# Kernel tuning notes

Hardware: AMD Instinct MI355X
Metric: run time of the kernel (lower is better)

## Reference

```python
import jax, jax.numpy as jnp
import numpy as np

QLEN, BSZ, HID, NH, HD = 512, 8, 1024, 16, 64
PLEN = 2 * QLEN
SCALE = 1.0 / (HD ** 0.5)
BIG_NUM = 1e30
EPS = 1e-5


def _rel_shift(x, klen):
    # x: [b, n, i, j] -> shifted [b, n, i, klen], same raw-reshape trick as torch.
    b, n, i, j = x.shape
    x = x.reshape(b, n, j, i)[:, :, 1:, :]
    x = x.reshape(b, n, i, j - 1)
    return x[:, :, :, :klen]


def setup_inputs() -> dict:
    key = jax.random.key(0)
    ks = jax.random.split(key, 12)
    s = jnp.float32(0.02)
    return {
        "hidden_states": jax.random.normal(ks[0], (QLEN, BSZ, HID), jnp.float32),
        "position_embed": jax.random.normal(ks[1], (PLEN, BSZ, HID), jnp.float32),
        "segment_embed": jax.random.uniform(ks[2], (QLEN, QLEN, BSZ, 2), jnp.float32),
        "attn_mask": jnp.zeros((QLEN, QLEN, BSZ, 1), jnp.float32),
        "q": jax.random.normal(ks[3], (HID, NH, HD), jnp.float32) * s,
        "k": jax.random.normal(ks[4], (HID, NH, HD), jnp.float32) * s,
        "v": jax.random.normal(ks[5], (HID, NH, HD), jnp.float32) * s,
        "r": jax.random.normal(ks[6], (HID, NH, HD), jnp.float32) * s,
        "o": jax.random.normal(ks[7], (HID, NH, HD), jnp.float32) * s,
        "r_w_bias": jax.random.normal(ks[8], (NH, HD), jnp.float32) * s,
        "r_r_bias": jax.random.normal(ks[9], (NH, HD), jnp.float32) * s,
        "r_s_bias": jax.random.normal(ks[10], (NH, HD), jnp.float32) * s,
        "seg_mat": jax.random.normal(ks[11], (2, NH, HD), jnp.float32) * s,
        "ln_gamma": jnp.ones((HID,), jnp.float32),
        "ln_beta": jnp.zeros((HID,), jnp.float32),
    }


def reference(hidden_states, position_embed, segment_embed, attn_mask,
              q, k, v, r, o, r_w_bias, r_r_bias, r_s_bias, seg_mat,
              ln_gamma, ln_beta):
    query = jnp.einsum('ibh,hnd->ibnd', hidden_states, q)
    key_ = jnp.einsum('ibh,hnd->ibnd', hidden_states, k)
    value = jnp.einsum('ibh,hnd->ibnd', hidden_states, v)
    key_r = jnp.einsum('ibh,hnd->ibnd', position_embed, r)

    # content score
    ac = jnp.einsum('ibnd,jbnd->bnij', query + r_w_bias, key_)
    # relative position score with rel_shift
    bd = jnp.einsum('ibnd,jbnd->bnij', query + r_r_bias, key_r)
    bd = _rel_shift(bd, ac.shape[3])
    # segment score
    ef = jnp.einsum('ibnd,snd->ibns', query + r_s_bias, seg_mat)
    ef = jnp.einsum('ijbs,ibns->bnij', segment_embed, ef)

    attn_score = (ac + bd + ef) * SCALE
    attn_score = attn_score - BIG_NUM * jnp.transpose(attn_mask, (2, 3, 0, 1))
    attn_prob = jax.nn.softmax(attn_score, axis=-1)  # dropout is identity in eval

    attn_out = jnp.einsum('bnij,jbnd->ibnd', attn_prob, value)
    attn_out = jnp.einsum('ibnd,hnd->ibh', attn_out, o)

    x = attn_out + hidden_states
    mu = jnp.mean(x, axis=-1, keepdims=True)
    var = jnp.mean((x - mu) ** 2, axis=-1, keepdims=True)
    return (x - mu) * jax.lax.rsqrt(var + EPS) * ln_gamma + ln_beta
```

## Files before the change

kernel.cpp:

```cpp
#include <hip/hip_runtime.h>
#include <hip/hip_bf16.h>

#define I_LEN 512
#define BSZ   8
#define HIDN  1024
#define NHEAD 16
#define HDIM  64
#define PLEN_ 1024
#define SCALE_F 0.125f
#define BIGNUM 1e30f
#define LN_EPS 1e-5f

typedef unsigned int   u32;
typedef unsigned short u16;
typedef __attribute__((ext_vector_type(8))) short bf16x8;
typedef __attribute__((ext_vector_type(4))) float f32x4;

__device__ __forceinline__ float bflo(u32 w) { return __uint_as_float(w << 16); }
__device__ __forceinline__ float bfhi(u32 w) { return __uint_as_float(w & 0xffff0000u); }
__device__ __forceinline__ u16 f2bf(float x) {
  u32 u = __float_as_uint(x);
  return (u16)((u + 0x7fffu + ((u >> 16) & 1u)) >> 16);
}
__device__ __forceinline__ void bf8_to_f(const uint4 v, float* f) {
  f[0] = bflo(v.x); f[1] = bfhi(v.x);
  f[2] = bflo(v.y); f[3] = bfhi(v.y);
  f[4] = bflo(v.z); f[5] = bfhi(v.z);
  f[6] = bflo(v.w); f[7] = bfhi(v.w);
}

#define GLOAD_LDS16(gp, lp) __builtin_amdgcn_global_load_lds( \
    (const __attribute__((address_space(1))) void*)(gp),      \
    (__attribute__((address_space(3))) void*)(lp), 16, 0, 0)

__device__ __forceinline__ void setrans_body(int i, int j,
    const float* __restrict__ sege, const float* __restrict__ amask,
    u16* __restrict__ SE4, u16* __restrict__ MK) {
  const float* sp = &sege[((size_t)i * 512 + j) * 16];
  const float* mp = &amask[((size_t)i * 512 + j) * 8];
  float se[16], mk[8];
#pragma unroll
  for (int q = 0; q < 4; ++q) {
    const float4 f = *(const float4*)(sp + q * 4);
    se[q * 4 + 0] = f.x; se[q * 4 + 1] = f.y; se[q * 4 + 2] = f.z; se[q * 4 + 3] = f.w;
  }
#pragma unroll
  for (int q = 0; q < 2; ++q) {
    const float4 f = *(const float4*)(mp + q * 4);
    mk[q * 4 + 0] = f.x; mk[q * 4 + 1] = f.y; mk[q * 4 + 2] = f.z; mk[q * 4 + 3] = f.w;
  }
#pragma unroll
  for (int b = 0; b < 8; ++b) {
    const u32 pk = (u32)f2bf(se[b * 2]) | ((u32)f2bf(se[b * 2 + 1]) << 16);
    const size_t plane = ((size_t)b * 512 + i) * 512 + j;
    *(u32*)&SE4[plane * 2] = pk;
    MK[plane] = f2bf(BIGNUM * mk[b]);
  }
}

__global__ __launch_bounds__(256)
void setrans_kernel(const float* __restrict__ sege, const float* __restrict__ amask,
                    u16* __restrict__ SE4, u16* __restrict__ MK) {
  const int blk = blockIdx.x;
  setrans_body(blk & 511, (blk >> 9) * 256 + threadIdx.x, sege, amask, SE4, MK);
}

__global__ __launch_bounds__(256)
void prep_kernel(const float* __restrict__ W0, const float* __restrict__ W1,
                 const float* __restrict__ W2, const float* __restrict__ W3,
                 u16* __restrict__ T0, u16* __restrict__ T1,
                 u16* __restrict__ T2, u16* __restrict__ T3,
                 const float* __restrict__ hidden, const float* __restrict__ ow,
                 u16* __restrict__ Hb, u16* __restrict__ Wob) {
  const int blk = blockIdx.x;
  const int t = threadIdx.x;
  if (blk >= 1024) {
    const size_t i = (size_t)(blk - 1024) * 256 + t;
    const float* src; u16* dst; size_t off;
    if (i < 524288) { src = hidden; dst = Hb;  off = i * 8; }
    else            { src = ow;     dst = Wob; off = (i - 524288) * 8; }
    const float4 a = *(const float4*)&src[off];
    const float4 b = *(const float4*)&src[off + 4];
    ushort4 o0, o1;
    o0.x = f2bf(a.x); o0.y = f2bf(a.y); o0.z = f2bf(a.z); o0.w = f2bf(a.w);
    o1.x = f2bf(b.x); o1.y = f2bf(b.y); o1.z = f2bf(b.z); o1.w = f2bf(b.w);
    *(ushort4*)&dst[off] = o0;
    *(ushort4*)&dst[off + 4] = o1;
    return;
  }
  __shared__ u16 tile[64][72];
  const int x = blk & 15, y = (blk >> 4) & 15, z = blk >> 8;
  const float* W = (z == 0) ? W0 : ((z == 1) ? W1 : ((z == 2) ? W2 : W3));
  u16* T = (z == 0) ? T0 : ((z == 1) ? T1 : ((z == 2) ? T2 : T3));
  const int h0 = y * 64, nd0 = x * 64;
  {
    const int hr = t >> 2, c0 = (t & 3) * 16;
#pragma unroll
    for (int q = 0; q < 4; ++q) {
      const float4 f = *(const float4*)&W[(size_t)(h0 + hr) * 1024 + nd0 + c0 + q * 4];
      tile[hr][c0 + q * 4 + 0] = f2bf(f.x);
      tile[hr][c0 + q * 4 + 1] = f2bf(f.y);
      tile[hr][c0 + q * 4 + 2] = f2bf(f.z);
      tile[hr][c0 + q * 4 + 3] = f2bf(f.w);
    }
  }
  __syncthreads();
  const int ndr = t >> 2, hc0 = (t & 3) * 16;
  union { u16 us[16]; uint4 qv[2]; } o;
#pragma unroll
  for (int e = 0; e < 16; ++e) o.us[e] = tile[hc0 + e][ndr];
  uint4* dst = (uint4*)&T[(size_t)(nd0 + ndr) * 1024 + h0 + hc0];
  dst[0] = o.qv[0]; dst[1] = o.qv[1];
}

__global__ __launch_bounds__(256)
void proj_gemm(const u16* __restrict__ Hb, const float* __restrict__ pos,
               const u16* __restrict__ Wqt, const u16* __restrict__ Wkt,
               const u16* __restrict__ Wvt, const u16* __restrict__ Wrt,
               u16* __restrict__ Qh, u16* __restrict__ Kf,
               u16* __restrict__ Vh, u16* __restrict__ Krf,
               const float* __restrict__ sege, const float* __restrict__ amask,
               u16* __restrict__ SE4, u16* __restrict__ MK) {
  if (blockIdx.x >= 1280) {
    const int sid = blockIdx.x - 1280;
    setrans_body(sid & 511, (sid >> 9) * 256 + threadIdx.x, sege, amask, SE4, MK);
    return;
  }
  constexpr int K = 1024;
  __shared__ union {
    struct { u16 As[2 * 8192]; u16 Bs[2 * 8192]; } st;
    u16 epi[4][64 * 68];
    u16 epiK[128 * 137];
  } sm;
  u16* As = sm.st.As;
  u16* Bs = sm.st.Bs;
  const int id = blockIdx.x;
  const int low = id & 7;
  const int rest = id >> 3;
  const int bx = rest & 7;
  const int grp = low + 8 * (rest >> 3);
  const int by = grp & 31;
  const int z = grp >> 5;
  const u16* Bt; u16* C;
  if (z == 0)      { Bt = Wqt; C = Qh;  }
  else if (z == 1) { Bt = Wkt; C = Kf;  }
  else if (z == 2) { Bt = Wvt; C = Vh;  }
  else if (z == 3) { Bt = Wrt; C = Krf; }
  else             { Bt = Wrt; C = Krf; }
  const float* Apos = pos + (size_t)((z == 4) ? 4096 : 0) * 1024;
  const int bm = by * 128, bn = bx * 128;
  const int tid = threadIdx.x, wv = tid >> 6, lane = tid & 63;
  const int l15 = lane & 15, g = lane >> 4;
  const int wr = wv >> 1, wc = wv & 1;

#define STAGE_B_P(BUF, K0)                                                    \
  _Pragma("unroll")                                                           \
  for (int p = 0; p < 4; ++p) {                                               \
    const int unit = (wv * 4 + p) * 64 + lane;                                \
    const int row = unit >> 3, up = unit & 7, cc = up ^ (row & 7);            \
    GLOAD_LDS16(&Bt[(size_t)(bn + row) * K + (K0) + cc * 8],                  \
                &Bs[(BUF) * 8192 + unit * 8]);                                \
  }
#define STAGE_A16_P(BUF, K0)                                                  \
  _Pragma("unroll")                                                           \
  for (int p = 0; p < 4; ++p) {                                               \
    const int unit = (wv * 4 + p) * 64 + lane;                                \
    const int row = unit >> 3, up = unit & 7, cc = up ^ (row & 7);            \
    GLOAD_LDS16(&Hb[(size_t)(bm + row) * K + (K0) + cc * 8],                  \
                &As[(BUF) * 8192 + unit * 8]);                                \
  }
#define STAGE_A32_P(BUF, K0)                                                  \
  _Pragma("unroll")                                                           \
  for (int p = 0; p < 4; ++p) {                                               \
    const int unit = p * 256 + tid;                                           \
    const int row = unit >> 3, up = unit & 7, cc = up ^ (row & 7);            \
    const float* src = &Apos[(size_t)(bm + row) * K + (K0) + cc * 8];         \
    const float4 f0 = *(const float4*)src;                                    \
    const float4 f1 = *(const float4*)(src + 4);                              \
    ushort4 h0, h1;                                                           \
    h0.x = f2bf(f0.x); h0.y = f2bf(f0.y); h0.z = f2bf(f0.z); h0.w = f2bf(f0.w); \
    h1.x = f2bf(f1.x); h1.y = f2bf(f1.y); h1.z = f2bf(f1.z); h1.w = f2bf(f1.w); \
    *(ushort4*)&As[(BUF) * 8192 + unit * 8] = h0;                             \
    *(ushort4*)&As[(BUF) * 8192 + unit * 8 + 4] = h1;                         \
  }
#define COMPUTE_TILE(CUR)                                                     \
  {                                                                           \
    const u16* Ac = &As[(CUR) * 8192];                                        \
    const u16* Bc = &Bs[(CUR) * 8192];                                        \
    _Pragma("unroll")                                                         \
    for (int h = 0; h < 2; ++h) {                                             \
      bf16x8 af[4], bfv[4];                                                   \
      _Pragma("unroll")                                                       \
      for (int m = 0; m < 4; ++m) {                                           \
        const int row = wr * 64 + m * 16 + l15;                               \
        af[m] = *(const bf16x8*)&Ac[row * 64 + ((h * 4 + g) ^ (row & 7)) * 8];\
      }                                                                       \
      _Pragma("unroll")                                                       \
      for (int n = 0; n < 4; ++n) {                                           \
        const int col = wc * 64 + n * 16 + l15;                               \
        bfv[n] = *(const bf16x8*)&Bc[col * 64 + ((h * 4 + g) ^ (col & 7)) * 8];\
      }                                                                       \
      _Pragma("unroll")                                                       \
      for (int m = 0; m < 4; ++m)                                             \
        _Pragma("unroll")                                                     \
        for (int n = 0; n < 4; ++n)                                           \
          acc[m][n] = __builtin_amdgcn_mfma_f32_16x16x32_bf16(af[m], bfv[n],  \
                                                              acc[m][n], 0, 0, 0); \
    }                                                                         \
  }

  f32x4 acc[4][4];
#pragma unroll
  for (int m = 0; m < 4; ++m)
#pragma unroll
    for (int n = 0; n < 4; ++n) acc[m][n] = (f32x4){0.f, 0.f, 0.f, 0.f};

  if (z < 3) {
    STAGE_B_P(0, 0);
    STAGE_A16_P(0, 0);
    int cur = 0;
    for (int t = 0; t < 16; ++t) {
      if (t < 15) {
        const int k1 = (t + 1) * 64;
        STAGE_B_P(cur ^ 1, k1);
        STAGE_A16_P(cur ^ 1, k1);
        asm volatile("s_waitcnt vmcnt(8)" ::: "memory");
      } else {
        asm volatile("s_waitcnt vmcnt(0)" ::: "memory");
      }
      __builtin_amdgcn_s_barrier();
      __builtin_amdgcn_sched_barrier(0);
      COMPUTE_TILE(cur);
      __builtin_amdgcn_s_barrier();
      cur ^= 1;
    }
  } else {
    STAGE_B_P(0, 0);
    STAGE_A32_P(0, 0);
    __syncthreads();
    int cur = 0;
    for (int t = 0; t < 16; ++t) {
      if (t < 15) {
        const int k1 = (t + 1) * 64;
        STAGE_B_P(cur ^ 1, k1);
        STAGE_A32_P(cur ^ 1, k1);
      }
      COMPUTE_TILE(cur);
      __syncthreads();
      cur ^= 1;
    }
  }

  if (z == 1 || z >= 3) {
    u16* E128 = sm.epiK;
#pragma unroll
    for (int m = 0; m < 4; ++m)
#pragma unroll
      for (int nf = 0; nf < 4; ++nf)
#pragma unroll
        for (int r = 0; r < 4; ++r)
          E128[(wr * 64 + m * 16 + g * 4 + r) * 137 + wc * 64 + nf * 16 + l15] =
              f2bf(acc[m][nf][r]);
    __syncthreads();
    const int tK = (z == 1) ? by : (by + ((z == 4) ? 32 : 0));
    const int TS = (z == 1) ? 32 : 64;
#pragma unroll
    for (int q = 0; q < 8; ++q) {
      const int rid = wv * 8 + q;
      const int n_loc = rid >> 4, b_ = (rid >> 1) & 7, h = rid & 1;
      union { u16 us[8]; uint4 qv; } o;
#pragma unroll
      for (int e = 0; e < 8; ++e)
        o.us[e] = E128[(l15 * 8 + b_) * 137 + n_loc * 64 + h * 32 + g * 8 + e];
      const int head = bx * 2 + n_loc;
      const size_t base = (((size_t)(b_ * 16 + head) * TS + tK) * 2 + h) * 512 + lane * 8;
      *(uint4*)&C[base] = o.qv;
    }
  } else {
    u16* slice = sm.epi[wv];
    __syncthreads();
#pragma unroll
    for (int m = 0; m < 4; ++m)
#pragma unroll
      for (int nf = 0; nf < 4; ++nf)
#pragma unroll
        for (int r = 0; r < 4; ++r)
          slice[(m * 16 + g * 4 + r) * 68 + nf * 16 + l15] = f2bf(acc[m][nf][r]);
#pragma unroll
    for (int it = 0; it < 8; ++it) {
      const int rl = it * 8 + (lane >> 3);
      const int cl = (lane & 7) * 8;
      const ushort4 a = *(const ushort4*)&slice[rl * 68 + cl];
      const ushort4 b2 = *(const ushort4*)&slice[rl * 68 + cl + 4];
      const int row = bm + wr * 64 + rl;
      const int col = bn + wc * 64 + cl;
      const size_t idx = ((size_t)((row & 7) * 16 + (col >> 6)) * 512 + (row >> 3)) * 64 + (col & 63);
      *(ushort4*)&C[idx] = a;
      *(ushort4*)&C[idx + 4] = b2;
    }
  }
}

__global__ __launch_bounds__(256)
void post_kernel(u16* __restrict__ V, const u16* __restrict__ Qh,
                 const float* __restrict__ rsb, const float* __restrict__ segm,
                 float* __restrict__ E) {
  const int blk = blockIdx.x;
  const int t = threadIdx.x;
  if (blk >= 1024) {
    const int gt = (blk - 1024) * 256 + t;
    const int i = gt >> 7, bb = (gt >> 4) & 7, n = gt & 15;
    const size_t base = (((size_t)bb * 16 + n) * 512 + i) * 64;
    float e0 = 0.f, e1 = 0.f;
#pragma unroll
    for (int u8 = 0; u8 < 8; ++u8) {
      const uint4 qv = *(const uint4*)&Qh[base + u8 * 8];
      float qf[8];
      bf8_to_f(qv, qf);
#pragma unroll
      for (int w = 0; w < 8; ++w) {
        const int d = u8 * 8 + w;
        const float q = qf[w] + rsb[n * HDIM + d];
        e0 += q * segm[n * HDIM + d];
        e1 += q * segm[HIDN + n * HDIM + d];
      }
    }
    E[(size_t)gt * 2 + 0] = e0;
    E[(size_t)gt * 2 + 1] = e1;
    return;
  }
  __shared__ u16 tile[64][72];
  const int bn = blk & 127, slab = blk >> 7;
  const size_t base = ((size_t)bn * 8 + slab) * 4096;
  {
    const int jl = t >> 2, c0 = (t & 3) * 16;
    const uint4 v0 = *(const uint4*)&V[base + jl * 64 + c0];
    const uint4 v1 = *(const uint4*)&V[base + jl * 64 + c0 + 8];
    *(uint4*)&tile[jl][c0] = v0;
    *(uint4*)&tile[jl][c0 + 8] = v1;
  }
  __syncthreads();
  const int lane = t & 63, g = lane >> 4, l15 = lane & 15;
#pragma unroll
  for (int w = 0; w < 2; ++w) {
    const int run = w * 4 + (t >> 6);
    const int c = run >> 1, h = run & 1;
    union { u16 us[8]; uint4 qv; } o;
#pragma unroll
    for (int e = 0; e < 8; ++e) o.us[e] = tile[h * 32 + g * 8 + e][16 * c + l15];
    *(uint4*)&V[base + run * 512 + lane * 8] = o.qv;
  }
}

__global__ __launch_bounds__(256)
void attn_mfma(const u16* __restrict__ Qh, const u16* __restrict__ Kf,
               const u16* __restrict__ Vf, const u16* __restrict__ Krf,
               const float* __restrict__ E, const u16* __restrict__ SE4,
               const u16* __restrict__ MK, const float* __restrict__ rwb,
               const float* __restrict__ rrb, u16* __restrict__ AOb) {
  __shared__ u16 Pl[4][16 * 64];
  const int id = blockIdx.x;
  const int b = id & 7, n = (id >> 3) & 15;
  const int i0 = (id >> 7) * 64;
  const int bn = b * 16 + n;
  const int t = threadIdx.x, wv = t >> 6, lane = t & 63;
  const int l15 = lane & 15, g = lane >> 4;
  const int irow0 = i0 + wv * 16;
  u16* Pw = Pl[wv];
  const int bn64 = bn * 64;

  bf16x8 qcf[2], qrf[2];
#pragma unroll
  for (int h = 0; h < 2; ++h) {
    const int d0 = 32 * h + g * 8;
    const uint4 qv = *(const uint4*)&Qh[((size_t)bn * 512 + irow0 + l15) * 64 + d0];
    float qf[8]; bf8_to_f(qv, qf);
    union { u16 us[8]; bf16x8 v; } ua, ub;
#pragma unroll
    for (int w = 0; w < 8; ++w) {
      ua.us[w] = f2bf((qf[w] + rwb[n * HDIM + d0 + w]) * SCALE_F);
      ub.us[w] = f2bf((qf[w] + rrb[n * HDIM + d0 + w]) * SCALE_F);
    }
    qcf[h] = ua.v; qrf[h] = ub.v;
  }

  float e0v[4], e1v[4], lrun[4];
  f32x4 accO[4];
#pragma unroll
  for (int r = 0; r < 4; ++r) {
    const int i = irow0 + 4 * g + r;
    const float2 ee = *(const float2*)&E[((size_t)(i * BSZ + b) * NHEAD + n) * 2];
    e0v[r] = ee.x * SCALE_F; e1v[r] = ee.y * SCALE_F;
    lrun[r] = 0.f;
  }
#pragma unroll
  for (int c = 0; c < 4; ++c) accO[c] = (f32x4){0.f, 0.f, 0.f, 0.f};

  for (int jb = 0; jb < I_LEN; jb += 64) {
    f32x4 S[4];
#pragma unroll
    for (int c = 0; c < 4; ++c) S[c] = (f32x4){0.f, 0.f, 0.f, 0.f};
#pragma unroll
    for (int c = 0; c < 4; ++c) {
      const u16* kp = &Kf[(((size_t)bn * 32 + (jb >> 4) + c) * 2) * 512 + lane * 8];
      S[c] = __builtin_amdgcn_mfma_f32_16x16x32_bf16(qcf[0], *(const bf16x8*)kp, S[c], 0, 0, 0);
      S[c] = __builtin_amdgcn_mfma_f32_16x16x32_bf16(qcf[1], *(const bf16x8*)(kp + 512), S[c], 0, 0, 0);
    }
    const int tb = (jb + 496 - irow0) >> 4;
    f32x4 T[5];
#pragma unroll
    for (int c = 0; c < 5; ++c) T[c] = (f32x4){0.f, 0.f, 0.f, 0.f};
#pragma unroll
    for (int c = 0; c < 5; ++c) {
      const u16* kp = &Krf[(((size_t)bn * 64 + tb + c) * 2) * 512 + lane * 8];
      T[c] = __builtin_amdgcn_mfma_f32_16x16x32_bf16(qrf[0], *(const bf16x8*)kp, T[c], 0, 0, 0);
      T[c] = __builtin_amdgcn_mfma_f32_16x16x32_bf16(qrf[1], *(const bf16x8*)(kp + 512), T[c], 0, 0, 0);
    }
    u32 sev[4][4]; u16 mkv[4][4];
#pragma unroll
    for (int c = 0; c < 4; ++c)
#pragma unroll
      for (int r = 0; r < 4; ++r) {
        const size_t plane = ((size_t)b * 512 + (irow0 + 4 * g + r)) * 512 + jb + 16 * c + l15;
        sev[c][r] = *(const u32*)&SE4[plane * 2];
        mkv[c][r] = MK[plane];
      }
    bf16x8 vf[4][2];
#pragma unroll
    for (int c = 0; c < 4; ++c) {
      const u16* vp = &Vf[((((size_t)bn * 8 + (jb >> 6)) * 4 + c) * 2) * 512 + lane * 8];
      vf[c][0] = *(const bf16x8*)vp;
      vf[c][1] = *(const bf16x8*)(vp + 512);
    }
    float bd[4][4];
#pragma unroll
    for (int r = 0; r < 4; ++r) {
      const int ii = 4 * g + r;
      const int pos = (lane & 48) | ((l15 - ii) & 15);
      float bp[5];
#pragma unroll
      for (int c = 0; c < 5; ++c) bp[c] = __shfl(T[c][r], pos, 64);
      const bool sel = l15 >= ii;
#pragma unroll
      for (int c = 0; c < 4; ++c) bd[c][r] = sel ? bp[c + 1] : bp[c];
    }
#pragma unroll
    for (int c = 0; c < 4; ++c)
#pragma unroll
      for (int r = 0; r < 4; ++r) {
        const u32 sev_ = sev[c][r];
        const float s = S[c][r] + bd[c][r] + bflo(sev_) * e0v[r] + bfhi(sev_) * e1v[r]
                        - bflo((u32)mkv[c][r]);
        const float p = __expf(s);
        S[c][r] = p;
        lrun[r] += p;
      }
#pragma unroll
    for (int c = 0; c < 4; ++c)
#pragma unroll
      for (int r = 0; r < 4; ++r) {
        const int ii = 4 * g + r;
        Pw[ii * 64 + ((16 * c + l15) ^ ((ii & 7) << 3))] = f2bf(S[c][r]);
      }
    const bf16x8 pa0 = *(const bf16x8*)&Pw[l15 * 64 + ((g * 8) ^ ((l15 & 7) << 3))];
    const bf16x8 pa1 = *(const bf16x8*)&Pw[l15 * 64 + ((32 + g * 8) ^ ((l15 & 7) << 3))];
#pragma unroll
    for (int c = 0; c < 4; ++c) {
      accO[c] = __builtin_amdgcn_mfma_f32_16x16x32_bf16(pa0, vf[c][0], accO[c], 0, 0, 0);
      accO[c] = __builtin_amdgcn_mfma_f32_16x16x32_bf16(pa1, vf[c][1], accO[c], 0, 0, 0);
    }
  }
#pragma unroll
  for (int r = 0; r < 4; ++r) {
#pragma unroll
    for (int o = 1; o < 16; o <<= 1) lrun[r] += __shfl_xor(lrun[r], o);
  }
#pragma unroll
  for (int c = 0; c < 4; ++c)
#pragma unroll
    for (int r = 0; r < 4; ++r) {
      const int ii = 4 * g + r;
      AOb[(size_t)(irow0 + ii) * 8192 + bn64 + 16 * c + l15] = f2bf(accO[c][r] / lrun[r]);
    }
}

__global__ __launch_bounds__(256)
void oproj_gemm(const u16* __restrict__ A, const u16* __restrict__ Wob,
                const float* __restrict__ Res, float* __restrict__ C) {
  constexpr int K = 1024;
  __shared__ u16 As[2 * 4096];
  __shared__ u16 Bs[2 * 8192];
  const int id = blockIdx.x;
  const int low = id & 7;
  const int rest = id >> 3;
  const int bx = rest & 7;
  const int by = low + 8 * (rest >> 3);
  const int bm = by * 64, bn = bx * 128;
  const int tid = threadIdx.x, wv = tid >> 6, lane = tid & 63;
  const int l15 = lane & 15, g = lane >> 4;
  const int wr = wv >> 1, wc = wv & 1;

#define STAGE_O(BUF, K0)                                                      \
  _Pragma("unroll")                                                           \
  for (int p = 0; p < 2; ++p) {                                               \
    const int unit = (wv * 2 + p) * 64 + lane;                                \
    const int row = unit >> 3, up = unit & 7, cc = up ^ (row & 7);            \
    GLOAD_LDS16(&A[(size_t)(bm + row) * K + (K0) + cc * 8],                   \
                &As[(BUF) * 4096 + unit * 8]);                                \
  }                                                                           \
  _Pragma("unroll")                                                           \
  for (int p = 0; p < 4; ++p) {                                               \
    const int unit = (wv * 4 + p) * 64 + lane;                                \
    const int row = unit >> 3, up = unit & 7, cc = up ^ (row & 7);            \
    GLOAD_LDS16(&Wob[(size_t)(bn + row) * K + (K0) + cc * 8],                 \
                &Bs[(BUF) * 8192 + unit * 8]);                                \
  }

  f32x4 acc[2][4];
#pragma unroll
  for (int m = 0; m < 2; ++m)
#pragma unroll
    for (int n = 0; n < 4; ++n) acc[m][n] = (f32x4){0.f, 0.f, 0.f, 0.f};

  STAGE_O(0, 0);
  int cur = 0;
  for (int t = 0; t < 16; ++t) {
    if (t < 15) {
      STAGE_O(cur ^ 1, (t + 1) * 64);
      asm volatile("s_waitcnt vmcnt(6)" ::: "memory");
    } else {
      asm volatile("s_waitcnt vmcnt(0)" ::: "memory");
    }
    __builtin_amdgcn_s_barrier();
    __builtin_amdgcn_sched_barrier(0);
    const u16* Ac = &As[cur * 4096];
    const u16* Bc = &Bs[cur * 8192];
#pragma unroll
    for (int h = 0; h < 2; ++h) {
      bf16x8 af[2], bfv[4];
#pragma unroll
      for (int m = 0; m < 2; ++m) {
        const int row = wr * 32 + m * 16 + l15;
        af[m] = *(const bf16x8*)&Ac[row * 64 + ((h * 4 + g) ^ (row & 7)) * 8];
      }
#pragma unroll
      for (int n = 0; n < 4; ++n) {
        const int col = wc * 64 + n * 16 + l15;
        bfv[n] = *(const bf16x8*)&Bc[col * 64 + ((h * 4 + g) ^ (col & 7)) * 8];
      }
#pragma unroll
      for (int m = 0; m < 2; ++m)
#pragma unroll
        for (int n = 0; n < 4; ++n)
          acc[m][n] = __builtin_amdgcn_mfma_f32_16x16x32_bf16(af[m], bfv[n], acc[m][n], 0, 0, 0);
    }
    __builtin_amdgcn_s_barrier();
    cur ^= 1;
  }
#pragma unroll
  for (int m = 0; m < 2; ++m) {
    const int row0 = bm + wr * 32 + m * 16 + g * 4;
#pragma unroll
    for (int nf = 0; nf < 4; ++nf) {
      const int col = bn + wc * 64 + nf * 16 + l15;
#pragma unroll
      for (int r = 0; r < 4; ++r) {
        const int row = row0 + r;
        C[(size_t)row * 1024 + col] = acc[m][nf][r] + Res[(size_t)row * 1024 + col];
      }
    }
  }
}

__global__ __launch_bounds__(256)
void ln_kernel(const float* __restrict__ X, const float* __restrict__ gam,
               const float* __restrict__ bet, float* __restrict__ out) {
  const int row = blockIdx.x, t = threadIdx.x;
  const float4 x4 = *(const float4*)&X[(size_t)row * HIDN + t * 4];
  float s  = x4.x + x4.y + x4.z + x4.w;
  float sq = x4.x * x4.x + x4.y * x4.y + x4.z * x4.z + x4.w * x4.w;
#pragma unroll
  for (int o = 32; o >= 1; o >>= 1) { s += __shfl_xor(s, o); sq += __shfl_xor(sq, o); }
  __shared__ float red[8];
  const int wv = t >> 6;
  if ((t & 63) == 0) { red[wv * 2] = s; red[wv * 2 + 1] = sq; }
  __syncthreads();
  s  = red[0] + red[2] + red[4] + red[6];
  sq = red[1] + red[3] + red[5] + red[7];
  const float mu  = s * (1.f / HIDN);
  const float var = sq * (1.f / HIDN) - mu * mu;
  const float rs  = rsqrtf(var + LN_EPS);
  const float4 g4 = *(const float4*)&gam[t * 4];
  const float4 b4 = *(const float4*)&bet[t * 4];
  float4 o4;
  o4.x = (x4.x - mu) * rs * g4.x + b4.x;
  o4.y = (x4.y - mu) * rs * g4.y + b4.y;
  o4.z = (x4.z - mu) * rs * g4.z + b4.z;
  o4.w = (x4.w - mu) * rs * g4.w + b4.w;
  *(float4*)&out[(size_t)row * HIDN + t * 4] = o4;
}

extern "C" void kernel_launch(void* const* d_in, const int* in_sizes, int n_in,
                              void* d_out, int out_size, void* d_ws, size_t ws_size,
                              hipStream_t stream) {
  (void)in_sizes; (void)n_in; (void)out_size;
  const float* hidden = (const float*)d_in[0];
  const float* pos    = (const float*)d_in[1];
  const float* sege   = (const float*)d_in[2];
  const float* amask  = (const float*)d_in[3];
  const float* qw     = (const float*)d_in[4];
  const float* kw     = (const float*)d_in[5];
  const float* vw     = (const float*)d_in[6];
  const float* rw     = (const float*)d_in[7];
  const float* ow     = (const float*)d_in[8];
  const float* rwb    = (const float*)d_in[9];
  const float* rrb    = (const float*)d_in[10];
  const float* rsb    = (const float*)d_in[11];
  const float* segm   = (const float*)d_in[12];
  const float* gam    = (const float*)d_in[13];
  const float* bet    = (const float*)d_in[14];
  float* out = (float*)d_out;
  char* ws = (char*)d_ws;

  const size_t MiB = 1ull << 20;
  u16*   Wqt = (u16*)(ws);
  u16*   Wkt = (u16*)(ws + 2 * MiB);
  u16*   Wvt = (u16*)(ws + 4 * MiB);
  u16*   Wrt = (u16*)(ws + 6 * MiB);
  u16*   AOb = (u16*)(ws);
  u16*   Qh  = (u16*)(ws + 8 * MiB);
  u16*   Kf  = (u16*)(ws + 16 * MiB);
  u16*   Vf  = (u16*)(ws + 24 * MiB);
  u16*   Krf = (u16*)(ws + 32 * MiB);
  float* X   = (float*)(ws + 32 * MiB);
  u16*   Hb  = (u16*)(ws + 48 * MiB);
  u16*   SE4_lo = (u16*)(ws + 48 * MiB);
  u16*   MK  = (u16*)(ws + 56 * MiB);
  float* E   = (float*)(ws + 60 * MiB);
  u16*   Wob = (u16*)(ws + 60 * MiB + 512 * 1024);
  u16*   SE4_hi = (u16*)(ws + 62 * MiB + 512 * 1024);

  const bool merged = ws_size >= (70 * MiB + 512 * 1024 + 4096);
  u16* SE4 = merged ? SE4_hi : SE4_lo;

  prep_kernel<<<3584, 256, 0, stream>>>(qw, kw, vw, rw, Wqt, Wkt, Wvt, Wrt,
                                        hidden, ow, Hb, Wob);
  proj_gemm<<<merged ? 2304 : 1280, 256, 0, stream>>>(
      Hb, pos, Wqt, Wkt, Wvt, Wrt, Qh, Kf, Vf, Krf, sege, amask, SE4, MK);
  if (!merged)
    setrans_kernel<<<1024, 256, 0, stream>>>(sege, amask, SE4, MK);
  post_kernel<<<1280, 256, 0, stream>>>(Vf, Qh, rsb, segm, E);
  attn_mfma<<<1024, 256, 0, stream>>>(Qh, Kf, Vf, Krf, E, SE4, MK, rwb, rrb, AOb);
  oproj_gemm<<<512, 256, 0, stream>>>(AOb, Wob, hidden, X);
  ln_kernel<<<4096, 256, 0, stream>>>(X, gam, bet, out);
}
```

Before: 164.5 us.

## Move segment/mask transpose and pos bf16 conversion into prep kernel

Moves the segment-embed/mask transpose work from the projection GEMM launch into the prep kernel. When the workspace is large enough, the prep kernel also converts position_embed to bf16, so the positional projection can use the async bf16 LDS load path instead of converting fp32 inline. In the attention loop, the SE4/MK and V fragment loads are hoisted ahead of the score MFMAs to overlap memory latency with compute. The cost is an extra bf16 buffer write and read, plus a prep kernel that now has more blocks and more branching. The old fallback path that used SE4_lo and a separate kernel is dropped, so SE4 now always sits at the high offset regardless of workspace size.

```diff
diff --git a/kernel.cpp b/kernel.cpp
--- a/kernel.cpp
+++ b/kernel.cpp
@@ -59,21 +59,33 @@
 }
 
 __global__ __launch_bounds__(256)
-void setrans_kernel(const float* __restrict__ sege, const float* __restrict__ amask,
-                    u16* __restrict__ SE4, u16* __restrict__ MK) {
-  const int blk = blockIdx.x;
-  setrans_body(blk & 511, (blk >> 9) * 256 + threadIdx.x, sege, amask, SE4, MK);
-}
-
-__global__ __launch_bounds__(256)
 void prep_kernel(const float* __restrict__ W0, const float* __restrict__ W1,
                  const float* __restrict__ W2, const float* __restrict__ W3,
                  u16* __restrict__ T0, u16* __restrict__ T1,
                  u16* __restrict__ T2, u16* __restrict__ T3,
                  const float* __restrict__ hidden, const float* __restrict__ ow,
-                 u16* __restrict__ Hb, u16* __restrict__ Wob) {
+                 u16* __restrict__ Hb, u16* __restrict__ Wob,
+                 const float* __restrict__ sege, const float* __restrict__ amask,
+                 u16* __restrict__ SE4, u16* __restrict__ MK,
+                 const float* __restrict__ pos, u16* __restrict__ Pb) {
   const int blk = blockIdx.x;
   const int t = threadIdx.x;
+  if (blk >= 4608) {
+    const size_t off = ((size_t)(blk - 4608) * 256 + t) * 8;
+    const float4 a = *(const float4*)&pos[off];
+    const float4 b = *(const float4*)&pos[off + 4];
+    ushort4 o0, o1;
+    o0.x = f2bf(a.x); o0.y = f2bf(a.y); o0.z = f2bf(a.z); o0.w = f2bf(a.w);
+    o1.x = f2bf(b.x); o1.y = f2bf(b.y); o1.z = f2bf(b.z); o1.w = f2bf(b.w);
+    *(ushort4*)&Pb[off] = o0;
+    *(ushort4*)&Pb[off + 4] = o1;
+    return;
+  }
+  if (blk >= 3584) {
+    const int sid = blk - 3584;
+    setrans_body(sid & 511, (sid >> 9) * 256 + t, sege, amask, SE4, MK);
+    return;
+  }
   if (blk >= 1024) {
     const size_t i = (size_t)(blk - 1024) * 256 + t;
     const float* src; u16* dst; size_t off;
@@ -115,17 +127,11 @@
 
 __global__ __launch_bounds__(256)
 void proj_gemm(const u16* __restrict__ Hb, const float* __restrict__ pos,
+               const u16* __restrict__ Pb,
                const u16* __restrict__ Wqt, const u16* __restrict__ Wkt,
                const u16* __restrict__ Wvt, const u16* __restrict__ Wrt,
                u16* __restrict__ Qh, u16* __restrict__ Kf,
-               u16* __restrict__ Vh, u16* __restrict__ Krf,
-               const float* __restrict__ sege, const float* __restrict__ amask,
-               u16* __restrict__ SE4, u16* __restrict__ MK) {
-  if (blockIdx.x >= 1280) {
-    const int sid = blockIdx.x - 1280;
-    setrans_body(sid & 511, (sid >> 9) * 256 + threadIdx.x, sege, amask, SE4, MK);
-    return;
-  }
+               u16* __restrict__ Vh, u16* __restrict__ Krf) {
   constexpr int K = 1024;
   __shared__ union {
     struct { u16 As[2 * 8192]; u16 Bs[2 * 8192]; } st;
@@ -147,7 +153,9 @@
   else if (z == 2) { Bt = Wvt; C = Vh;  }
   else if (z == 3) { Bt = Wrt; C = Krf; }
   else             { Bt = Wrt; C = Krf; }
-  const float* Apos = pos + (size_t)((z == 4) ? 4096 : 0) * 1024;
+  const int rowoff = (z == 4) ? 4096 : 0;
+  const float* Apos = pos + (size_t)rowoff * 1024;
+  const u16* A16 = (z < 3) ? Hb : (Pb ? Pb + (size_t)rowoff * 1024 : nullptr);
   const int bm = by * 128, bn = bx * 128;
   const int tid = threadIdx.x, wv = tid >> 6, lane = tid & 63;
   const int l15 = lane & 15, g = lane >> 4;
@@ -166,7 +174,7 @@
   for (int p = 0; p < 4; ++p) {                                               \
     const int unit = (wv * 4 + p) * 64 + lane;                                \
     const int row = unit >> 3, up = unit & 7, cc = up ^ (row & 7);            \
-    GLOAD_LDS16(&Hb[(size_t)(bm + row) * K + (K0) + cc * 8],                  \
+    GLOAD_LDS16(&A16[(size_t)(bm + row) * K + (K0) + cc * 8],                 \
                 &As[(BUF) * 8192 + unit * 8]);                                \
   }
 #define STAGE_A32_P(BUF, K0)                                                  \
@@ -215,7 +223,7 @@
 #pragma unroll
     for (int n = 0; n < 4; ++n) acc[m][n] = (f32x4){0.f, 0.f, 0.f, 0.f};
 
-  if (z < 3) {
+  if (A16) {
     STAGE_B_P(0, 0);
     STAGE_A16_P(0, 0);
     int cur = 0;
@@ -397,6 +405,22 @@
   for (int c = 0; c < 4; ++c) accO[c] = (f32x4){0.f, 0.f, 0.f, 0.f};
 
   for (int jb = 0; jb < I_LEN; jb += 64) {
+    u32 sev[4][4]; u16 mkv[4][4];
+#pragma unroll
+    for (int c = 0; c < 4; ++c)
+#pragma unroll
+      for (int r = 0; r < 4; ++r) {
+        const size_t plane = ((size_t)b * 512 + (irow0 + 4 * g + r)) * 512 + jb + 16 * c + l15;
+        sev[c][r] = *(const u32*)&SE4[plane * 2];
+        mkv[c][r] = MK[plane];
+      }
+    bf16x8 vf[4][2];
+#pragma unroll
+    for (int c = 0; c < 4; ++c) {
+      const u16* vp = &Vf[((((size_t)bn * 8 + (jb >> 6)) * 4 + c) * 2) * 512 + lane * 8];
+      vf[c][0] = *(const bf16x8*)vp;
+      vf[c][1] = *(const bf16x8*)(vp + 512);
+    }
     f32x4 S[4];
 #pragma unroll
     for (int c = 0; c < 4; ++c) S[c] = (f32x4){0.f, 0.f, 0.f, 0.f};
@@ -416,30 +440,14 @@
       T[c] = __builtin_amdgcn_mfma_f32_16x16x32_bf16(qrf[0], *(const bf16x8*)kp, T[c], 0, 0, 0);
       T[c] = __builtin_amdgcn_mfma_f32_16x16x32_bf16(qrf[1], *(const bf16x8*)(kp + 512), T[c], 0, 0, 0);
     }
-    u32 sev[4][4]; u16 mkv[4][4];
-#pragma unroll
-    for (int c = 0; c < 4; ++c)
-#pragma unroll
-      for (int r = 0; r < 4; ++r) {
-        const size_t plane = ((size_t)b * 512 + (irow0 + 4 * g + r)) * 512 + jb + 16 * c + l15;
-        sev[c][r] = *(const u32*)&SE4[plane * 2];
-        mkv[c][r] = MK[plane];
-      }
-    bf16x8 vf[4][2];
-#pragma unroll
-    for (int c = 0; c < 4; ++c) {
-      const u16* vp = &Vf[((((size_t)bn * 8 + (jb >> 6)) * 4 + c) * 2) * 512 + lane * 8];
-      vf[c][0] = *(const bf16x8*)vp;
-      vf[c][1] = *(const bf16x8*)(vp + 512);
-    }
     float bd[4][4];
 #pragma unroll
     for (int r = 0; r < 4; ++r) {
       const int ii = 4 * g + r;
-      const int pos = (lane & 48) | ((l15 - ii) & 15);
+      const int pos_ = (lane & 48) | ((l15 - ii) & 15);
       float bp[5];
 #pragma unroll
-      for (int c = 0; c < 5; ++c) bp[c] = __shfl(T[c][r], pos, 64);
+      for (int c = 0; c < 5; ++c) bp[c] = __shfl(T[c][r], pos_, 64);
       const bool sel = l15 >= ii;
 #pragma unroll
       for (int c = 0; c < 4; ++c) bd[c][r] = sel ? bp[c + 1] : bp[c];
@@ -634,21 +642,18 @@
   u16*   Krf = (u16*)(ws + 32 * MiB);
   float* X   = (float*)(ws + 32 * MiB);
   u16*   Hb  = (u16*)(ws + 48 * MiB);
-  u16*   SE4_lo = (u16*)(ws + 48 * MiB);
   u16*   MK  = (u16*)(ws + 56 * MiB);
   float* E   = (float*)(ws + 60 * MiB);
   u16*   Wob = (u16*)(ws + 60 * MiB + 512 * 1024);
-  u16*   SE4_hi = (u16*)(ws + 62 * MiB + 512 * 1024);
-
-  const bool merged = ws_size >= (70 * MiB + 512 * 1024 + 4096);
-  u16* SE4 = merged ? SE4_hi : SE4_lo;
-
-  prep_kernel<<<3584, 256, 0, stream>>>(qw, kw, vw, rw, Wqt, Wkt, Wvt, Wrt,
-                                        hidden, ow, Hb, Wob);
-  proj_gemm<<<merged ? 2304 : 1280, 256, 0, stream>>>(
-      Hb, pos, Wqt, Wkt, Wvt, Wrt, Qh, Kf, Vf, Krf, sege, amask, SE4, MK);
-  if (!merged)
-    setrans_kernel<<<1024, 256, 0, stream>>>(sege, amask, SE4, MK);
+  u16*   SE4 = (u16*)(ws + 62 * MiB + 512 * 1024);
+  const bool fullTier = ws_size >= (86 * MiB + 512 * 1024 + 4096);
+  u16*   Pb  = fullTier ? (u16*)(ws + 70 * MiB + 512 * 1024) : nullptr;
+
+  prep_kernel<<<fullTier ? 8704 : 4608, 256, 0, stream>>>(
+      qw, kw, vw, rw, Wqt, Wkt, Wvt, Wrt, hidden, ow, Hb, Wob,
+      sege, amask, SE4, MK, pos, Pb);
+  proj_gemm<<<1280, 256, 0, stream>>>(Hb, pos, Pb, Wqt, Wkt, Wvt, Wrt,
+                                      Qh, Kf, Vf, Krf);
   post_kernel<<<1280, 256, 0, stream>>>(Vf, Qh, rsb, segm, E);
   attn_mfma<<<1024, 256, 0, stream>>>(Qh, Kf, Vf, Krf, E, SE4, MK, rwb, rrb, AOb);
   oproj_gemm<<<512, 256, 0, stream>>>(AOb, Wob, hidden, X);
```

After: 161.3 us. 1.02x faster.
